# Performance work log

Measured on AMD Instinct MI355X. Metric: run time of the kernel, lower is better.

Reference implementation:

```python
import jax, jax.numpy as jnp
import numpy as np

B, S, DM = 4, 2048, 1024
H, HD = 16, 64  # num_heads, head_dimension


def setup_inputs() -> dict:
    key = jax.random.key(0)
    ks = jax.random.split(key, 11)
    s = 0.02
    return {
        "queries": jax.random.normal(ks[0], (B, S, DM), dtype=jnp.float32),
        "keys": jax.random.normal(ks[1], (B, S, DM), dtype=jnp.float32),
        "values": jax.random.normal(ks[2], (B, S, DM), dtype=jnp.float32),
        # projection params, stored [in, out] (transpose of torch Linear weight)
        "Wq": jax.random.normal(ks[3], (DM, H * HD), dtype=jnp.float32) * s,
        "bq": jnp.zeros((H * HD,), dtype=jnp.float32),
        "Wk": jax.random.normal(ks[4], (DM, H * HD), dtype=jnp.float32) * s,
        "bk": jnp.zeros((H * HD,), dtype=jnp.float32),
        "Wv": jax.random.normal(ks[5], (DM, H * HD), dtype=jnp.float32) * s,
        "bv": jnp.zeros((H * HD,), dtype=jnp.float32),
        "Wo": jax.random.normal(ks[6], (H * HD, DM), dtype=jnp.float32) * s,
        "bo": jnp.zeros((DM,), dtype=jnp.float32),
    }


def reference(queries, keys, values, Wq, bq, Wk, bk, Wv, bv, Wo, bo):
    b, s, _ = queries.shape
    # project and split heads: [b, s, H*HD] -> [b, H, s, HD]
    def split(x):
        return x.reshape(b, s, H, HD).transpose(0, 2, 1, 3)
    q = split(queries @ Wq + bq)
    k = split(keys @ Wk + bk)
    v = split(values @ Wv + bv)
    # raw scores [b, H, sq, sk]
    attn = jnp.einsum("bhqd,bhkd->bhqk", q, k)
    # FAITHFUL to source: mask is a no-op (masked_fill result discarded);
    # softmax over axis=2 (the QUERY axis), then scaled by 1/sqrt(HD) after.
    attn = jax.nn.softmax(attn, axis=2) / jnp.sqrt(jnp.float32(HD))
    out = jnp.einsum("bhqk,bhkd->bhqd", attn, v)  # [b, H, s, HD]
    out = out.transpose(0, 2, 1, 3).reshape(b, s, H * HD)
    return out @ Wo + bo
```

## Files before the change

### kernel.cpp

```cpp
#include <hip/hip_runtime.h>
#include <cstddef>


typedef unsigned short u16t;
typedef __attribute__((ext_vector_type(8))) short short8;
typedef __attribute__((ext_vector_type(4))) float floatx4;

#define MFMA16(a, b, c) __builtin_amdgcn_mfma_f32_16x16x32_bf16((a), (b), (c), 0, 0, 0)
#define GLDS16(g, l)                                                        \
  __builtin_amdgcn_global_load_lds(                                         \
      (const __attribute__((address_space(1))) unsigned int*)(g),           \
      (__attribute__((address_space(3))) unsigned int*)(l), 16, 0, 0)

#if __has_builtin(__builtin_amdgcn_exp2f)
#define EXP2(x) __builtin_amdgcn_exp2f(x)
#else
#define EXP2(x) __expf(0.69314718f * (x))
#endif

static __device__ __forceinline__ u16t f2bf(float f) {
  union { float f; unsigned u; } v; v.f = f;
  unsigned r = v.u + 0x7FFFu + ((v.u >> 16) & 1u);
  return (u16t)(r >> 16);
}
static __device__ __forceinline__ unsigned pack2(float hi, float lo) {
  union { float f; unsigned u; } a, b; a.f = hi; b.f = lo;
  return __builtin_amdgcn_perm(a.u + 0x8000u, b.u + 0x8000u, 0x07060302u);
}

static __device__ __forceinline__ int swz(int row, int col) {
  return (((col >> 3) ^ (row & 7)) << 3) | (col & 7);
}

#define SEQ    2048
#define NHEAD  16
#define HDIM   64
#define DMODEL 1024

__global__ __launch_bounds__(256)
void wt_kernel(const float* __restrict__ W0, const float* __restrict__ W1,
               const float* __restrict__ W2, const float* __restrict__ W3,
               u16t* __restrict__ T0, u16t* __restrict__ T1,
               u16t* __restrict__ T2, u16t* __restrict__ T3) {
  int id = blockIdx.x * 256 + threadIdx.x;
  int wsel = id >> 17;
  int r = id & 131071;
  int n = r & 1023;
  int k0 = (r >> 10) << 3;
  const float* W = wsel == 0 ? W0 : wsel == 1 ? W1 : wsel == 2 ? W2 : W3;
  u16t* T = wsel == 0 ? T0 : wsel == 1 ? T1 : wsel == 2 ? T2 : T3;
  const float* src = W + (size_t)k0 * 1024 + n;
  float f[8];
#pragma unroll
  for (int i = 0; i < 8; ++i) f[i] = src[(size_t)i * 1024];
  uint4 p;
  p.x = pack2(f[1], f[0]); p.y = pack2(f[3], f[2]);
  p.z = pack2(f[5], f[4]); p.w = pack2(f[7], f[6]);
  *(uint4*)&T[(size_t)n * 1024 + (k0 & ~63) + swz(n, k0 & 63)] = p;
}

template <int MODE>
__global__ __launch_bounds__(256)
void gemm_bt(const void* __restrict__ Ap0, const void* __restrict__ Ap1,
             const u16t* __restrict__ BT0, const u16t* __restrict__ BT1,
             const float* __restrict__ bias0, const float* __restrict__ bias1,
             void* __restrict__ Cp0, void* __restrict__ Cp1,
             float sc0, float sc1, const float* __restrict__ sscv) {
  constexpr int K = 1024;
  __shared__ __align__(16) u16t lA[128 * 64];
  __shared__ __align__(16) u16t lB[128 * 64];
  const int z = blockIdx.z;
  const void* Ap = z ? Ap1 : Ap0;
  const u16t* BT = z ? BT1 : BT0;
  const float* bias = z ? bias1 : bias0;
  void* Cp = z ? Cp1 : Cp0;
  const float qsc = z ? sc1 : sc0;
  const int tid = threadIdx.x;
  const int lane = tid & 63, w = tid >> 6;
  const int wm = w >> 1, wn = w & 1;
  const int lrow = lane & 15, lq = lane >> 4;
  const int m0 = blockIdx.y * 128, n0 = blockIdx.x * 128;

  floatx4 acc[4][4];
#pragma unroll
  for (int i = 0; i < 4; ++i)
#pragma unroll
    for (int j = 0; j < 4; ++j) acc[i][j] = {0.f, 0.f, 0.f, 0.f};

  for (int kb = 0; kb < K; kb += 64) {
    if constexpr (MODE == 1) {
      const u16t* Ag = (const u16t*)Ap;
#pragma unroll
      for (int i = 0; i < 4; ++i) {
        int chunk = w * 4 + i;
        int off = chunk * 1024 + lane * 16;
        int r = off >> 7, ib = off & 127;
        GLDS16(Ag + (size_t)(m0 + r) * K + kb + (ib >> 1), &lA[chunk * 512]);
      }
    } else {
      const float* Ag = (const float*)Ap;
#pragma unroll
      for (int i = 0; i < 8; ++i) {
        int e = (i * 256 + tid) * 4;
        int r = e >> 6, c = e & 63;
        const float* src = Ag + (size_t)(m0 + r) * K + kb + c;
        uint2 p;
        p.x = pack2(src[1], src[0]);
        p.y = pack2(src[3], src[2]);
        *(uint2*)&lA[r * 64 + swz(r, c)] = p;
      }
    }
#pragma unroll
    for (int i = 0; i < 4; ++i) {
      int chunk = w * 4 + i;
      int off = chunk * 1024 + lane * 16;
      int r = off >> 7, ib = off & 127;
      GLDS16(BT + (size_t)(n0 + r) * K + kb + (ib >> 1), &lB[chunk * 512]);
    }
    __syncthreads();
#pragma unroll
    for (int kk = 0; kk < 2; ++kk) {
      short8 af[4], bfr[4];
#pragma unroll
      for (int t = 0; t < 4; ++t) {
        int ar = wm * 64 + t * 16 + lrow;
        af[t] = *(const short8*)&lA[ar * 64 + swz(ar, kk * 32 + lq * 8)];
      }
#pragma unroll
      for (int t = 0; t < 4; ++t) {
        int br = wn * 64 + t * 16 + lrow;
        bfr[t] = *(const short8*)&lB[br * 64 + swz(br, kk * 32 + lq * 8)];
      }
#pragma unroll
      for (int i = 0; i < 4; ++i)
#pragma unroll
        for (int j = 0; j < 4; ++j)
          acc[i][j] = MFMA16(af[i], bfr[j], acc[i][j]);
    }
    __syncthreads();
  }

  float bvv[4];
#pragma unroll
  for (int j = 0; j < 4; ++j) bvv[j] = bias[n0 + wn * 64 + j * 16 + lrow];
  const int h = (n0 + wn * 64) >> 6;
#pragma unroll
  for (int i = 0; i < 4; ++i) {
#pragma unroll
    for (int r = 0; r < 4; ++r) {
      int rg = m0 + wm * 64 + i * 16 + lq * 4 + r;
      int b = rg >> 11, s = rg & 2047;
      float rs;
      if constexpr (MODE == 2) rs = sscv[(size_t)(b * NHEAD + h) * SEQ + s];
      else                     rs = qsc;
#pragma unroll
      for (int j = 0; j < 4; ++j) {
        int cg = n0 + wn * 64 + j * 16 + lrow;
        float v = acc[i][j][r] + bvv[j];
        if constexpr (MODE == 1) {
          ((float*)Cp)[(size_t)rg * 1024 + cg] = v;
        } else {
          v *= rs;
          int d = cg & 63;
          size_t bh = (size_t)(b * NHEAD + h);
          if constexpr (MODE == 0)
            ((u16t*)Cp)[(bh * SEQ + s) * HDIM + swz(s, d)] = f2bf(v);
          else
            ((u16t*)Cp)[(bh * HDIM + d) * SEQ + (s & ~127) + swz(d, s & 127)] = f2bf(v);
        }
      }
    }
  }
}

__global__ __launch_bounds__(256)
void stats_kernel(const u16t* __restrict__ Qb, const u16t* __restrict__ Kb,
                  float* __restrict__ ss) {
  __shared__ __align__(16) u16t lK[128 * 64];
  __shared__ __align__(16) u16t lQ[128 * 64];
  const int tid = threadIdx.x, lane = tid & 63, w = tid >> 6;
  const int lrow = lane & 15, lq = lane >> 4;
  const int bh = blockIdx.y;
  const int c0 = blockIdx.x * 128;
  const u16t* Kbase = Kb + (size_t)bh * (SEQ * HDIM);
  const u16t* Qbase = Qb + (size_t)bh * (SEQ * HDIM);

#pragma unroll
  for (int i = 0; i < 4; ++i) {
    int chunk = w * 4 + i;
    GLDS16(Kbase + (size_t)c0 * HDIM + chunk * 512 + lane * 8, &lK[chunk * 512]);
  }

  short8 bfK[4];
  float lcur[2] = {0.f, 0.f};

  for (int q0 = 0; q0 < SEQ; q0 += 128) {
#pragma unroll
    for (int i = 0; i < 4; ++i) {
      int chunk = w * 4 + i;
      GLDS16(Qbase + (size_t)q0 * HDIM + chunk * 512 + lane * 8, &lQ[chunk * 512]);
    }
    __syncthreads();
    if (q0 == 0) {
#pragma unroll
      for (int nt = 0; nt < 2; ++nt) {
        int kr = w * 32 + nt * 16 + lrow;
        bfK[nt * 2]     = *(const short8*)&lK[kr * 64 + swz(kr, lq * 8)];
        bfK[nt * 2 + 1] = *(const short8*)&lK[kr * 64 + swz(kr, lq * 8 + 32)];
      }
    }
#pragma unroll
    for (int mt = 0; mt < 8; ++mt) {
      int qr = mt * 16 + lrow;
      short8 af0 = *(const short8*)&lQ[qr * 64 + swz(qr, lq * 8)];
      short8 af1 = *(const short8*)&lQ[qr * 64 + swz(qr, lq * 8 + 32)];
#pragma unroll
      for (int nt = 0; nt < 2; ++nt) {
        floatx4 a = {0.f, 0.f, 0.f, 0.f};
        a = MFMA16(af0, bfK[nt * 2], a);
        a = MFMA16(af1, bfK[nt * 2 + 1], a);
        lcur[nt] += EXP2(a[0]) + EXP2(a[1]) + EXP2(a[2]) + EXP2(a[3]);
      }
    }
    __syncthreads();
  }
#pragma unroll
  for (int t = 0; t < 2; ++t) {
    float ll = lcur[t];
    ll += __shfl_xor(ll, 16);
    ll += __shfl_xor(ll, 32);
    lcur[t] = ll;
  }
  if (lane < 16) {
#pragma unroll
    for (int t = 0; t < 2; ++t) {
      int col = c0 + w * 32 + t * 16 + lane;
      ss[(size_t)bh * SEQ + col] = 1.f / (8.f * lcur[t]);
    }
  }
}

__global__ __launch_bounds__(256)
void attn_kernel(const u16t* __restrict__ Qb, const u16t* __restrict__ Kb,
                 const u16t* __restrict__ Vt, u16t* __restrict__ Hout) {
  __shared__ __align__(16) u16t lKP[128 * 64];
  __shared__ __align__(16) u16t lV[64 * 128];
  const int tid = threadIdx.x, lane = tid & 63, w = tid >> 6;
  const int lrow = lane & 15, lq = lane >> 4;
  const int bh = blockIdx.y, q0 = blockIdx.x * 64;
  const size_t hb = (size_t)bh * (SEQ * HDIM);

#pragma unroll
  for (int i = 0; i < 2; ++i) {
    int chunk = w * 2 + i;
    GLDS16(Qb + hb + (size_t)q0 * HDIM + chunk * 512 + lane * 8, &lKP[chunk * 512]);
  }
  __syncthreads();
  const int qr = w * 16 + lrow;
  short8 bq0 = *(const short8*)&lKP[qr * 64 + swz(qr, lq * 8)];
  short8 bq1 = *(const short8*)&lKP[qr * 64 + swz(qr, lq * 8 + 32)];
  __syncthreads();

  floatx4 ao[4];
#pragma unroll
  for (int t = 0; t < 4; ++t) ao[t] = {0.f, 0.f, 0.f, 0.f};

  for (int kt = 0; kt < 16; ++kt) {
    const int k0 = kt * 128;
#pragma unroll
    for (int i = 0; i < 4; ++i) {
      int chunk = w * 4 + i;
      GLDS16(Kb + hb + (size_t)k0 * HDIM + chunk * 512 + lane * 8, &lKP[chunk * 512]);
    }
#pragma unroll
    for (int i = 0; i < 4; ++i) {
      int chunk = w * 4 + i;
      int off = chunk * 1024 + lane * 16;
      int d = off >> 8, ib = off & 255;
      GLDS16(Vt + hb + ((size_t)d << 11) + k0 + (ib >> 1), &lV[chunk * 512]);
    }
    __syncthreads();

    floatx4 st[8];
#pragma unroll
    for (int nt = 0; nt < 8; ++nt) {
      int kr = nt * 16 + lrow;
      short8 ak0 = *(const short8*)&lKP[kr * 64 + swz(kr, lq * 8)];
      short8 ak1 = *(const short8*)&lKP[kr * 64 + swz(kr, lq * 8 + 32)];
      floatx4 a = {0.f, 0.f, 0.f, 0.f};
      a = MFMA16(ak0, bq0, a);
      a = MFMA16(ak1, bq1, a);
      st[nt] = a;
    }
    __syncthreads();

#pragma unroll
    for (int nt = 0; nt < 8; ++nt) {
      float p0 = EXP2(st[nt][0]);
      float p1 = EXP2(st[nt][1]);
      float p2 = EXP2(st[nt][2]);
      float p3 = EXP2(st[nt][3]);
      uint2 pk; pk.x = pack2(p1, p0); pk.y = pack2(p3, p2);
      *(uint2*)&lKP[qr * 128 + swz(qr, nt * 16 + lq * 4)] = pk;
    }
    {
      short8 ap[4];
#pragma unroll
      for (int kk = 0; kk < 4; ++kk)
        ap[kk] = *(const short8*)&lKP[qr * 128 + swz(qr, kk * 32 + lq * 8)];
#pragma unroll
      for (int nt = 0; nt < 4; ++nt) {
        int vr = nt * 16 + lrow;
#pragma unroll
        for (int kk = 0; kk < 4; ++kk) {
          short8 bv = *(const short8*)&lV[vr * 128 + swz(vr, kk * 32 + lq * 8)];
          ao[nt] = MFMA16(ap[kk], bv, ao[nt]);
        }
      }
    }
    __syncthreads();
  }

  const int b = bh >> 4, h = bh & 15;
#pragma unroll
  for (int nt = 0; nt < 4; ++nt) {
    int d = nt * 16 + lrow;
#pragma unroll
    for (int r = 0; r < 4; ++r) {
      int q = q0 + w * 16 + lq * 4 + r;
      Hout[((size_t)b * SEQ + q) * DMODEL + h * HDIM + swz(q, d)] = f2bf(ao[nt][r]);
    }
  }
}

extern "C" void kernel_launch(void* const* d_in, const int* in_sizes, int n_in,
                              void* d_out, int out_size, void* d_ws, size_t ws_size,
                              hipStream_t stream) {
  (void)in_sizes; (void)n_in; (void)out_size; (void)ws_size;
  const float* queries = (const float*)d_in[0];
  const float* keys    = (const float*)d_in[1];
  const float* values  = (const float*)d_in[2];
  const float* Wq = (const float*)d_in[3];
  const float* bq = (const float*)d_in[4];
  const float* Wk = (const float*)d_in[5];
  const float* bk = (const float*)d_in[6];
  const float* Wv = (const float*)d_in[7];
  const float* bv = (const float*)d_in[8];
  const float* Wo = (const float*)d_in[9];
  const float* bo = (const float*)d_in[10];

  char* ws = (char*)d_ws;
  const size_t MB = 1024 * 1024;
  u16t* Qb   = (u16t*)(ws + 0 * MB);
  u16t* Kb   = (u16t*)(ws + 16 * MB);
  u16t* Vt   = (u16t*)(ws + 32 * MB);
  u16t* Hout = (u16t*)(ws + 48 * MB);
  u16t* wqt  = (u16t*)(ws + 64 * MB);
  u16t* wkt  = (u16t*)(ws + 66 * MB);
  u16t* wvt  = (u16t*)(ws + 68 * MB);
  u16t* wot  = (u16t*)(ws + 70 * MB);
  float* ssc = (float*)(ws + 72 * MB);

  wt_kernel<<<2048, 256, 0, stream>>>(Wq, Wk, Wv, Wo, wqt, wkt, wvt, wot);

  gemm_bt<0><<<dim3(8, 64, 2), 256, 0, stream>>>(
      queries, keys, wqt, wkt, bq, bk, Qb, Kb, 1.44269504f, 1.0f, nullptr);

  stats_kernel<<<dim3(16, 64), 256, 0, stream>>>(Qb, Kb, ssc);

  gemm_bt<2><<<dim3(8, 64, 1), 256, 0, stream>>>(
      values, values, wvt, wvt, bv, bv, Vt, Vt, 1.0f, 1.0f, ssc);

  attn_kernel<<<dim3(32, 64), 256, 0, stream>>>(Qb, Kb, Vt, Hout);

  gemm_bt<1><<<dim3(8, 64, 1), 256, 0, stream>>>(
      Hout, Hout, wot, wot, bo, bo, d_out, d_out, 1.0f, 1.0f, nullptr);
}
```

Before: 452.3 us.

## Keep attention probabilities in registers and double queries per block

The attention kernel now feeds the exponentiated score fragments straight from registers into the PV MFMA as the A operand. It relies on a permuted column order in the V-transpose layout, written by the projection epilogue, and drops the LDS round trip plus one barrier per tile. Each block now handles 128 queries with two 16-row slices per wave, so every loaded K/V tile is reused twice. The grids for stats and attention are transposed so blocks sharing the same head run close together, which should improve L2 reuse. The costs are higher register pressure and half as many attention blocks.

After: 413.3 us. -8.6%, faster.

```diff
diff --git a/kernel.cpp b/kernel.cpp
--- a/kernel.cpp
+++ b/kernel.cpp
@@ -5,6 +5,7 @@
 typedef unsigned short u16t;
 typedef __attribute__((ext_vector_type(8))) short short8;
 typedef __attribute__((ext_vector_type(4))) float floatx4;
+typedef __attribute__((ext_vector_type(4))) unsigned int uintx4;
 
 #define MFMA16(a, b, c) __builtin_amdgcn_mfma_f32_16x16x32_bf16((a), (b), (c), 0, 0, 0)
 #define GLDS16(g, l)                                                        \
@@ -163,10 +164,14 @@
           v *= rs;
           int d = cg & 63;
           size_t bh = (size_t)(b * NHEAD + h);
-          if constexpr (MODE == 0)
+          if constexpr (MODE == 0) {
             ((u16t*)Cp)[(bh * SEQ + s) * HDIM + swz(s, d)] = f2bf(v);
-          else
-            ((u16t*)Cp)[(bh * HDIM + d) * SEQ + (s & ~127) + swz(d, s & 127)] = f2bf(v);
+          } else {
+            int sp = (s & ~31) | (((s >> 2) & 3) << 3) | (s & 3) |
+                     (((s >> 4) & 1) << 2);
+            ((u16t*)Cp)[(bh * HDIM + d) * SEQ + (s & ~127) + swz(d, sp & 127)] =
+                f2bf(v);
+          }
         }
       }
     }
@@ -180,8 +185,8 @@
   __shared__ __align__(16) u16t lQ[128 * 64];
   const int tid = threadIdx.x, lane = tid & 63, w = tid >> 6;
   const int lrow = lane & 15, lq = lane >> 4;
-  const int bh = blockIdx.y;
-  const int c0 = blockIdx.x * 128;
+  const int bh = blockIdx.x;
+  const int c0 = blockIdx.y * 128;
   const u16t* Kbase = Kb + (size_t)bh * (SEQ * HDIM);
   const u16t* Qbase = Qb + (size_t)bh * (SEQ * HDIM);
 
@@ -243,34 +248,40 @@
 __global__ __launch_bounds__(256)
 void attn_kernel(const u16t* __restrict__ Qb, const u16t* __restrict__ Kb,
                  const u16t* __restrict__ Vt, u16t* __restrict__ Hout) {
-  __shared__ __align__(16) u16t lKP[128 * 64];
+  __shared__ __align__(16) u16t lK[128 * 64];
   __shared__ __align__(16) u16t lV[64 * 128];
   const int tid = threadIdx.x, lane = tid & 63, w = tid >> 6;
   const int lrow = lane & 15, lq = lane >> 4;
-  const int bh = blockIdx.y, q0 = blockIdx.x * 64;
+  const int bh = blockIdx.x, q0 = blockIdx.y * 128;
   const size_t hb = (size_t)bh * (SEQ * HDIM);
 
 #pragma unroll
-  for (int i = 0; i < 2; ++i) {
-    int chunk = w * 2 + i;
-    GLDS16(Qb + hb + (size_t)q0 * HDIM + chunk * 512 + lane * 8, &lKP[chunk * 512]);
+  for (int i = 0; i < 4; ++i) {
+    int chunk = w * 4 + i;
+    GLDS16(Qb + hb + (size_t)q0 * HDIM + chunk * 512 + lane * 8, &lK[chunk * 512]);
   }
   __syncthreads();
-  const int qr = w * 16 + lrow;
-  short8 bq0 = *(const short8*)&lKP[qr * 64 + swz(qr, lq * 8)];
-  short8 bq1 = *(const short8*)&lKP[qr * 64 + swz(qr, lq * 8 + 32)];
+  short8 bq[2][2];
+#pragma unroll
+  for (int j = 0; j < 2; ++j) {
+    int qr = w * 32 + j * 16 + lrow;
+    bq[j][0] = *(const short8*)&lK[qr * 64 + swz(qr, lq * 8)];
+    bq[j][1] = *(const short8*)&lK[qr * 64 + swz(qr, lq * 8 + 32)];
+  }
   __syncthreads();
 
-  floatx4 ao[4];
-#pragma unroll
-  for (int t = 0; t < 4; ++t) ao[t] = {0.f, 0.f, 0.f, 0.f};
+  floatx4 ao[2][4];
+#pragma unroll
+  for (int j = 0; j < 2; ++j)
+#pragma unroll
+    for (int t = 0; t < 4; ++t) ao[j][t] = {0.f, 0.f, 0.f, 0.f};
 
   for (int kt = 0; kt < 16; ++kt) {
     const int k0 = kt * 128;
 #pragma unroll
     for (int i = 0; i < 4; ++i) {
       int chunk = w * 4 + i;
-      GLDS16(Kb + hb + (size_t)k0 * HDIM + chunk * 512 + lane * 8, &lKP[chunk * 512]);
+      GLDS16(Kb + hb + (size_t)k0 * HDIM + chunk * 512 + lane * 8, &lK[chunk * 512]);
     }
 #pragma unroll
     for (int i = 0; i < 4; ++i) {
@@ -281,41 +292,36 @@
     }
     __syncthreads();
 
-    floatx4 st[8];
-#pragma unroll
-    for (int nt = 0; nt < 8; ++nt) {
-      int kr = nt * 16 + lrow;
-      short8 ak0 = *(const short8*)&lKP[kr * 64 + swz(kr, lq * 8)];
-      short8 ak1 = *(const short8*)&lKP[kr * 64 + swz(kr, lq * 8 + 32)];
-      floatx4 a = {0.f, 0.f, 0.f, 0.f};
-      a = MFMA16(ak0, bq0, a);
-      a = MFMA16(ak1, bq1, a);
-      st[nt] = a;
-    }
-    __syncthreads();
-
-#pragma unroll
-    for (int nt = 0; nt < 8; ++nt) {
-      float p0 = EXP2(st[nt][0]);
-      float p1 = EXP2(st[nt][1]);
-      float p2 = EXP2(st[nt][2]);
-      float p3 = EXP2(st[nt][3]);
-      uint2 pk; pk.x = pack2(p1, p0); pk.y = pack2(p3, p2);
-      *(uint2*)&lKP[qr * 128 + swz(qr, nt * 16 + lq * 4)] = pk;
-    }
-    {
-      short8 ap[4];
-#pragma unroll
-      for (int kk = 0; kk < 4; ++kk)
-        ap[kk] = *(const short8*)&lKP[qr * 128 + swz(qr, kk * 32 + lq * 8)];
-#pragma unroll
-      for (int nt = 0; nt < 4; ++nt) {
-        int vr = nt * 16 + lrow;
-#pragma unroll
-        for (int kk = 0; kk < 4; ++kk) {
-          short8 bv = *(const short8*)&lV[vr * 128 + swz(vr, kk * 32 + lq * 8)];
-          ao[nt] = MFMA16(ap[kk], bv, ao[nt]);
-        }
+#pragma unroll
+    for (int kw = 0; kw < 4; ++kw) {
+      short8 ak[2][2];
+#pragma unroll
+      for (int t = 0; t < 2; ++t) {
+        int kr = (kw * 2 + t) * 16 + lrow;
+        ak[t][0] = *(const short8*)&lK[kr * 64 + swz(kr, lq * 8)];
+        ak[t][1] = *(const short8*)&lK[kr * 64 + swz(kr, lq * 8 + 32)];
+      }
+      short8 pa[2];
+#pragma unroll
+      for (int j = 0; j < 2; ++j) {
+        floatx4 s0 = {0.f, 0.f, 0.f, 0.f}, s1 = {0.f, 0.f, 0.f, 0.f};
+        s0 = MFMA16(ak[0][0], bq[j][0], s0);
+        s0 = MFMA16(ak[0][1], bq[j][1], s0);
+        s1 = MFMA16(ak[1][0], bq[j][0], s1);
+        s1 = MFMA16(ak[1][1], bq[j][1], s1);
+        uintx4 pw;
+        pw[0] = pack2(EXP2(s0[1]), EXP2(s0[0]));
+        pw[1] = pack2(EXP2(s0[3]), EXP2(s0[2]));
+        pw[2] = pack2(EXP2(s1[1]), EXP2(s1[0]));
+        pw[3] = pack2(EXP2(s1[3]), EXP2(s1[2]));
+        pa[j] = __builtin_bit_cast(short8, pw);
+      }
+#pragma unroll
+      for (int dt = 0; dt < 4; ++dt) {
+        int vr = dt * 16 + lrow;
+        short8 bv = *(const short8*)&lV[vr * 128 + swz(vr, kw * 32 + lq * 8)];
+        ao[0][dt] = MFMA16(pa[0], bv, ao[0][dt]);
+        ao[1][dt] = MFMA16(pa[1], bv, ao[1][dt]);
       }
     }
     __syncthreads();
@@ -323,14 +329,16 @@
 
   const int b = bh >> 4, h = bh & 15;
 #pragma unroll
-  for (int nt = 0; nt < 4; ++nt) {
-    int d = nt * 16 + lrow;
-#pragma unroll
-    for (int r = 0; r < 4; ++r) {
-      int q = q0 + w * 16 + lq * 4 + r;
-      Hout[((size_t)b * SEQ + q) * DMODEL + h * HDIM + swz(q, d)] = f2bf(ao[nt][r]);
-    }
-  }
+  for (int j = 0; j < 2; ++j)
+#pragma unroll
+    for (int dt = 0; dt < 4; ++dt) {
+      int d = dt * 16 + lrow;
+#pragma unroll
+      for (int r = 0; r < 4; ++r) {
+        int q = q0 + w * 32 + j * 16 + lq * 4 + r;
+        Hout[((size_t)b * SEQ + q) * DMODEL + h * HDIM + swz(q, d)] = f2bf(ao[j][dt][r]);
+      }
+    }
 }
 
 extern "C" void kernel_launch(void* const* d_in, const int* in_sizes, int n_in,
@@ -366,12 +374,12 @@
   gemm_bt<0><<<dim3(8, 64, 2), 256, 0, stream>>>(
       queries, keys, wqt, wkt, bq, bk, Qb, Kb, 1.44269504f, 1.0f, nullptr);
 
-  stats_kernel<<<dim3(16, 64), 256, 0, stream>>>(Qb, Kb, ssc);
+  stats_kernel<<<dim3(64, 16), 256, 0, stream>>>(Qb, Kb, ssc);
 
   gemm_bt<2><<<dim3(8, 64, 1), 256, 0, stream>>>(
       values, values, wvt, wvt, bv, bv, Vt, Vt, 1.0f, 1.0f, ssc);
 
-  attn_kernel<<<dim3(32, 64), 256, 0, stream>>>(Qb, Kb, Vt, Hout);
+  attn_kernel<<<dim3(64, 16), 256, 0, stream>>>(Qb, Kb, Vt, Hout);
 
   gemm_bt<1><<<dim3(8, 64, 1), 256, 0, stream>>>(
       Hout, Hout, wot, wot, bo, bo, d_out, d_out, 1.0f, 1.0f, nullptr);
```
